# Kernel optimization log

Measured on AMD Instinct MI355X. Metric: run time of the kernel, lower is better.

## Reference

```python
import jax, jax.numpy as jnp
import numpy as np

EPS = 1e-5
KP_EXTENT = 0.05


def _lrelu(x):
    return jnp.where(x >= 0, x, 0.1 * x)


def _bn(x, g, b, m, v):
    return g * (x - m) * jax.lax.rsqrt(v + EPS) + b


def setup_inputs() -> dict:
    key = jax.random.key(0)
    ks = jax.random.split(key, 20)
    N, K, P = 40000, 32, 15
    C_in, mid, C_out = 128, 64, 256
    inp = {}
    inp["features"] = jax.random.normal(ks[0], (N, C_in), dtype=jnp.float32)
    # points in a small cube so neighbor distances ~ KP_radius (0.06)
    inp["points"] = jax.random.uniform(ks[1], (N, 3), dtype=jnp.float32) * 0.1
    inp["neighbor_idx"] = jax.random.randint(ks[2], (N, K), 0, N, dtype=jnp.int32)
    # main path: Conv1D(in->mid) + BN
    inp["W1"] = jax.random.normal(ks[3], (C_in, mid), dtype=jnp.float32) * (1.0 / np.sqrt(C_in))
    inp["bn1_g"] = 1.0 + 0.1 * jax.random.normal(ks[4], (mid,), dtype=jnp.float32)
    inp["bn1_b"] = 0.1 * jax.random.normal(ks[5], (mid,), dtype=jnp.float32)
    inp["bn1_m"] = 0.1 * jax.random.normal(ks[6], (mid,), dtype=jnp.float32)
    inp["bn1_v"] = 0.5 + 0.5 * jax.random.uniform(ks[7], (mid,), dtype=jnp.float32)
    # KPConv: fixed kernel point positions in ball of radius 0.06, weights [P, mid, mid]
    inp["kernel_points"] = jax.random.normal(ks[8], (P, 3), dtype=jnp.float32) * 0.03
    inp["Wkp"] = jax.random.normal(ks[9], (P, mid, mid), dtype=jnp.float32) * (1.0 / np.sqrt(P * mid))
    # Conv1D(mid->out) + BN
    inp["W2"] = jax.random.normal(ks[10], (mid, C_out), dtype=jnp.float32) * (1.0 / np.sqrt(mid))
    inp["bn2_g"] = 1.0 + 0.1 * jax.random.normal(ks[11], (C_out,), dtype=jnp.float32)
    inp["bn2_b"] = 0.1 * jax.random.normal(ks[12], (C_out,), dtype=jnp.float32)
    inp["bn2_m"] = 0.1 * jax.random.normal(ks[13], (C_out,), dtype=jnp.float32)
    inp["bn2_v"] = 0.5 + 0.5 * jax.random.uniform(ks[14], (C_out,), dtype=jnp.float32)
    # shortcut Conv1D(in->out) + BN
    inp["Ws"] = jax.random.normal(ks[15], (C_in, C_out), dtype=jnp.float32) * (1.0 / np.sqrt(C_in))
    inp["bns_g"] = 1.0 + 0.1 * jax.random.normal(ks[16], (C_out,), dtype=jnp.float32)
    inp["bns_b"] = 0.1 * jax.random.normal(ks[17], (C_out,), dtype=jnp.float32)
    inp["bns_m"] = 0.1 * jax.random.normal(ks[18], (C_out,), dtype=jnp.float32)
    inp["bns_v"] = 0.5 + 0.5 * jax.random.uniform(ks[19], (C_out,), dtype=jnp.float32)
    return inp


def reference(features, points, neighbor_idx,
              W1, bn1_g, bn1_b, bn1_m, bn1_v,
              kernel_points, Wkp,
              W2, bn2_g, bn2_b, bn2_m, bn2_v,
              Ws, bns_g, bns_b, bns_m, bns_v):
    # --- main path ---
    # Conv1D: pointwise linear + BN(eval) + LeakyReLU
    x = _lrelu(_bn(features @ W1, bn1_g, bn1_b, bn1_m, bn1_v))  # [N, mid]
    # KPConvNeighbors (rigid KPConv, linear influence)
    f_n = x[neighbor_idx]                                # [N, K, mid] gather
    d = points[neighbor_idx] - points[:, None, :]        # [N, K, 3]
    diff = d[:, :, None, :] - kernel_points[None, None]  # [N, K, P, 3]
    dist = jnp.sqrt(jnp.sum(diff * diff, axis=-1))       # [N, K, P]
    h = jnp.maximum(0.0, 1.0 - dist / KP_EXTENT)         # influence [N, K, P]
    wf = jnp.einsum('nkp,nkc->npc', h, f_n)              # [N, P, mid]
    y = jnp.einsum('npc,pcd->nd', wf, Wkp)               # [N, mid]
    y = _lrelu(y)
    y = _lrelu(_bn(y @ W2, bn2_g, bn2_b, bn2_m, bn2_v))  # [N, C_out]
    # --- shortcut ---
    sc = _lrelu(_bn(features @ Ws, bns_g, bns_b, bns_m, bns_v))
    # residual add + final leaky relu
    return _lrelu(y + sc)
```

## Files before the change

kernel.cpp:

```cpp
#include <hip/hip_runtime.h>
#include <math.h>

#define EPSBN 1e-5f

constexpr int CIN  = 128;
constexpr int MID  = 64;
constexpr int COUT = 256;
constexpr int KNB  = 32;
constexpr int PKP  = 15;

constexpr int PSTR = 72;
constexpr int WROW = PKP * PSTR;
constexpr int YROW = 72;

typedef __bf16 v8bf  __attribute__((ext_vector_type(8)));
typedef float  f32x4 __attribute__((ext_vector_type(4)));

__device__ __forceinline__ float lrelu(float x) { return x >= 0.0f ? x : 0.1f * x; }

__device__ __forceinline__ void split1(float v, unsigned short& h, unsigned short& l) {
    __bf16 hb = (__bf16)v;
    float r = v - (float)hb;
    __bf16 lb = (__bf16)r;
    h = __builtin_bit_cast(unsigned short, hb);
    l = __builtin_bit_cast(unsigned short, lb);
}

__device__ __forceinline__ void split_frag8(const float* s, v8bf& hi, v8bf& lo) {
    #pragma unroll
    for (int j = 0; j < 8; ++j) {
        __bf16 hb = (__bf16)s[j];
        float r = s[j] - (float)hb;
        hi[j] = hb;
        lo[j] = (__bf16)r;
    }
}

__device__ __forceinline__ v8bf as_v8bf(uint4 u) {
    union { uint4 u; v8bf v; } X;
    X.u = u;
    return X.v;
}

__device__ __forceinline__ unsigned bf16_rne(float f) {
    unsigned u = __float_as_uint(f);
    return (u + 0x7fffu + ((u >> 16) & 1u)) >> 16;
}
__device__ __forceinline__ void split_pack8(const float* s, v8bf& hi, v8bf& lo) {
    unsigned h[8], l[8];
    #pragma unroll
    for (int j = 0; j < 8; ++j) {
        float a = s[j];
        unsigned hu = bf16_rne(a);
        float r = a - __uint_as_float(hu << 16);
        h[j] = hu;
        l[j] = bf16_rne(r);
    }
    union { uint4 u; v8bf v; } H, L;
    H.u = make_uint4(h[0] | (h[1] << 16), h[2] | (h[3] << 16),
                     h[4] | (h[5] << 16), h[6] | (h[7] << 16));
    L.u = make_uint4(l[0] | (l[1] << 16), l[2] | (l[3] << 16),
                     l[4] | (l[5] << 16), l[6] | (l[7] << 16));
    hi = H.v;
    lo = L.v;
}

__global__ __launch_bounds__(256) void prep(
    const float* __restrict__ Wkp, const float* __restrict__ W1,
    const float* __restrict__ Ws,  const float* __restrict__ W2,
    const float* __restrict__ g1, const float* __restrict__ b1,
    const float* __restrict__ m1, const float* __restrict__ v1,
    const float* __restrict__ gs, const float* __restrict__ bs,
    const float* __restrict__ ms, const float* __restrict__ vs,
    const float* __restrict__ g2, const float* __restrict__ b2,
    const float* __restrict__ m2, const float* __restrict__ v2,
    uint4* __restrict__ WkpPh, uint4* __restrict__ WkpPl,
    uint4* __restrict__ WcPh,  uint4* __restrict__ WcPl,
    uint4* __restrict__ W2Ph,  uint4* __restrict__ W2Pl,
    float* __restrict__ bnscale, float* __restrict__ bnshift)
{
    const int b = blockIdx.x, t = threadIdx.x;
    if (b < 30) {
        int gt = b * 256 + t;
        int lane = gt & 63, rest = gt >> 6;
        int nt = rest & 3, kt = rest >> 2;
        int col = nt * 16 + (lane & 15);
        int kbase = kt * 32 + ((lane >> 4) << 3);
        float tmp[8];
        #pragma unroll
        for (int j = 0; j < 8; ++j)
            tmp[j] = Wkp[(size_t)(kbase + j) * MID + col];
        v8bf hi, lo;
        split_pack8(tmp, hi, lo);
        union { v8bf v; uint4 u; } H, L; H.v = hi; L.v = lo;
        WkpPh[gt] = H.u; WkpPl[gt] = L.u;
    } else if (b < 50) {
        int gt = (b - 30) * 256 + t;
        int lane = gt & 63, rest = gt >> 6;
        int kt = rest / 20, nt = rest % 20;
        int c = nt * 16 + (lane & 15);
        int kbase = kt * 32 + ((lane >> 4) << 3);
        float tmp[8];
        #pragma unroll
        for (int j = 0; j < 8; ++j) {
            int k = kbase + j;
            tmp[j] = (c < 64) ? W1[(size_t)k * MID + c]
                              : Ws[(size_t)k * COUT + (c - 64)];
        }
        v8bf hi, lo;
        split_pack8(tmp, hi, lo);
        union { v8bf v; uint4 u; } H, L; H.v = hi; L.v = lo;
        WcPh[gt] = H.u; WcPl[gt] = L.u;
    } else if (b < 58) {
        int gt = (b - 50) * 256 + t;
        int lane = gt & 63, rest = gt >> 6;
        int kt = rest >> 4, nt = rest & 15;
        int col = nt * 16 + (lane & 15);
        int kbase = kt * 32 + ((lane >> 4) << 3);
        float tmp[8];
        #pragma unroll
        for (int j = 0; j < 8; ++j)
            tmp[j] = W2[(size_t)(kbase + j) * COUT + col];
        v8bf hi, lo;
        split_pack8(tmp, hi, lo);
        union { v8bf v; uint4 u; } H, L; H.v = hi; L.v = lo;
        W2Ph[gt] = H.u; W2Pl[gt] = L.u;
    } else {
        int v = (b - 58) * 256 + t;
        if (v < 576) {
            float g, bb, mm, vv;
            if (v < 64)       { g = g1[v]; bb = b1[v]; mm = m1[v]; vv = v1[v]; }
            else if (v < 320) { int c = v - 64;  g = gs[c]; bb = bs[c]; mm = ms[c]; vv = vs[c]; }
            else              { int c = v - 320; g = g2[c]; bb = b2[c]; mm = m2[c]; vv = v2[c]; }
            float s = g / sqrtf(vv + EPSBN);
            bnscale[v] = s;
            bnshift[v] = bb - mm * s;
        }
    }
}

__global__ __launch_bounds__(256) void k1_mfma(
    const float* __restrict__ F,
    const uint4* __restrict__ WcPh, const uint4* __restrict__ WcPl,
    const float* __restrict__ bnscale, const float* __restrict__ bnshift,
    unsigned* __restrict__ xp, float* __restrict__ scbuf)
{
    const int t = threadIdx.x;
    const int l = t & 63, w = t >> 6;
    const int n0 = blockIdx.x * 64;
    const int ntbase = blockIdx.y * 10;
    const int colr = l & 15, kg = l >> 4;
    const int arow = n0 + w * 16 + colr;
    const int k8 = kg * 8;

    const float* fr = F + (size_t)arow * CIN + k8;
    float4 av[4][2];
    #pragma unroll
    for (int kt = 0; kt < 4; ++kt) {
        av[kt][0] = *(const float4*)(fr + kt * 32);
        av[kt][1] = *(const float4*)(fr + kt * 32 + 4);
    }

    f32x4 acc[10];
    #pragma unroll
    for (int nt = 0; nt < 10; ++nt) acc[nt] = (f32x4){0.f, 0.f, 0.f, 0.f};

    #pragma unroll
    for (int kt = 0; kt < 4; ++kt) {
        float tmp[8] = {av[kt][0].x, av[kt][0].y, av[kt][0].z, av[kt][0].w,
                        av[kt][1].x, av[kt][1].y, av[kt][1].z, av[kt][1].w};
        v8bf ah, al;
        split_frag8(tmp, ah, al);
        #pragma unroll
        for (int nt = 0; nt < 10; ++nt) {
            int bidx = ((kt * 20 + ntbase + nt) << 6) + l;
            v8bf bh = as_v8bf(WcPh[bidx]);
            v8bf bl = as_v8bf(WcPl[bidx]);
            acc[nt] = __builtin_amdgcn_mfma_f32_16x16x32_bf16(ah, bh, acc[nt], 0, 0, 0);
            acc[nt] = __builtin_amdgcn_mfma_f32_16x16x32_bf16(al, bh, acc[nt], 0, 0, 0);
            acc[nt] = __builtin_amdgcn_mfma_f32_16x16x32_bf16(ah, bl, acc[nt], 0, 0, 0);
        }
    }

    const int rq = kg * 4;
    #pragma unroll
    for (int nt = 0; nt < 10; ++nt) {
        int col = (ntbase + nt) * 16 + colr;
        float sc = bnscale[col], sh = bnshift[col];
        #pragma unroll
        for (int r = 0; r < 4; ++r) {
            int row = n0 + w * 16 + rq + r;
            float val = lrelu(acc[nt][r] * sc + sh);
            if (col < 64) {
                unsigned short hu, lu;
                split1(val, hu, lu);
                xp[(size_t)row * MID + col] = ((unsigned)hu << 16) | lu;
            } else {
                scbuf[(size_t)row * COUT + (col - 64)] = val;
            }
        }
    }
}

__global__ __launch_bounds__(512) void k234_fused(
    const unsigned* __restrict__ xp,
    const float* __restrict__ pts,
    const int* __restrict__ nidx,
    const float* __restrict__ kpp,
    const uint4* __restrict__ WkpPh, const uint4* __restrict__ WkpPl,
    const uint4* __restrict__ W2Ph,  const uint4* __restrict__ W2Pl,
    const float* __restrict__ bnscale, const float* __restrict__ bnshift,
    const float* __restrict__ scbuf,
    float* __restrict__ out)
{
    __shared__ unsigned short wfsH[16 * WROW];
    __shared__ unsigned short wfsL[16 * WROW];
    __shared__ float         yP[4][16][17];
    __shared__ unsigned short yH[16 * YROW];
    __shared__ unsigned short yL[16 * YROW];

    const int t = threadIdx.x;
    const int l = t & 63, w = t >> 6;
    const int col = l & 15, kg = l >> 4;
    const int k8 = kg * 8;
    const int n0 = blockIdx.x * 16;

    float kx = 0.f, ky = 0.f, kz = 0.f;
    if (col < PKP) { kx = kpp[col * 3]; ky = kpp[col * 3 + 1]; kz = kpp[col * 3 + 2]; }

    for (int pt = 0; pt < 2; ++pt) {
        const int pl = w * 2 + pt;
        const int n  = n0 + pl;
        const float cx = pts[(size_t)n * 3];
        const float cy = pts[(size_t)n * 3 + 1];
        const float cz = pts[(size_t)n * 3 + 2];
        const int4 nba = ((const int4*)nidx)[(size_t)n * 8 + kg * 2];
        const int4 nbb = ((const int4*)nidx)[(size_t)n * 8 + kg * 2 + 1];
        int nb[8] = {nba.x, nba.y, nba.z, nba.w, nbb.x, nbb.y, nbb.z, nbb.w};

        unsigned u[8][4];
        #pragma unroll
        for (int j = 0; j < 8; ++j) {
            const unsigned* xr = xp + (size_t)nb[j] * MID + col;
            u[j][0] = xr[0];
            u[j][1] = xr[16];
            u[j][2] = xr[32];
            u[j][3] = xr[48];
        }

        float hv[8];
        #pragma unroll
        for (int j = 0; j < 8; ++j) {
            float ex = (pts[(size_t)nb[j] * 3]     - cx) - kx;
            float ey = (pts[(size_t)nb[j] * 3 + 1] - cy) - ky;
            float ez = (pts[(size_t)nb[j] * 3 + 2] - cz) - kz;
            float dist = sqrtf(ex * ex + ey * ey + ez * ez);
            float h = fmaxf(0.0f, 1.0f - dist * 20.0f);
            hv[j] = (col < PKP) ? h : 0.0f;
        }
        v8bf ah, al;
        split_frag8(hv, ah, al);

        #pragma unroll
        for (int nt = 0; nt < 4; ++nt) {
            unsigned bhW[4], blW[4];
            #pragma unroll
            for (int i = 0; i < 4; ++i) {
                unsigned u0 = u[2 * i][nt], u1 = u[2 * i + 1][nt];
                bhW[i] = (u1 & 0xFFFF0000u) | (u0 >> 16);
                blW[i] = (u1 << 16) | (u0 & 0xFFFFu);
            }
            v8bf bh = as_v8bf(make_uint4(bhW[0], bhW[1], bhW[2], bhW[3]));
            v8bf bl = as_v8bf(make_uint4(blW[0], blW[1], blW[2], blW[3]));
            f32x4 acc = {0.f, 0.f, 0.f, 0.f};
            acc = __builtin_amdgcn_mfma_f32_16x16x32_bf16(ah, bh, acc, 0, 0, 0);
            acc = __builtin_amdgcn_mfma_f32_16x16x32_bf16(al, bh, acc, 0, 0, 0);
            acc = __builtin_amdgcn_mfma_f32_16x16x32_bf16(ah, bl, acc, 0, 0, 0);
            #pragma unroll
            for (int r = 0; r < 4; ++r) {
                int p = kg * 4 + r;
                if (p < PKP) {
                    unsigned short hu, lu;
                    split1(acc[r], hu, lu);
                    int off = pl * WROW + p * PSTR + nt * 16 + col;
                    wfsH[off] = hu;
                    wfsL[off] = lu;
                }
            }
        }
    }
    __syncthreads();

    const int nt = w & 3;
    const int khalf = w >> 2;
    f32x4 a0 = {0.f, 0.f, 0.f, 0.f};
    f32x4 a1 = {0.f, 0.f, 0.f, 0.f};
    f32x4 a2 = {0.f, 0.f, 0.f, 0.f};
    #pragma unroll
    for (int i = 0; i < 15; ++i) {
        int kt = khalf * 15 + i;
        int koff = col * WROW + (kt >> 1) * PSTR + (kt & 1) * 32 + k8;
        v8bf ah = as_v8bf(*(const uint4*)&wfsH[koff]);
        v8bf al = as_v8bf(*(const uint4*)&wfsL[koff]);
        int bidx = ((kt << 2) + nt) * 64 + l;
        v8bf bh = as_v8bf(WkpPh[bidx]);
        v8bf bl = as_v8bf(WkpPl[bidx]);
        a0 = __builtin_amdgcn_mfma_f32_16x16x32_bf16(ah, bh, a0, 0, 0, 0);
        a1 = __builtin_amdgcn_mfma_f32_16x16x32_bf16(al, bh, a1, 0, 0, 0);
        a2 = __builtin_amdgcn_mfma_f32_16x16x32_bf16(ah, bl, a2, 0, 0, 0);
    }
    if (khalf == 1) {
        #pragma unroll
        for (int r = 0; r < 4; ++r)
            yP[nt][kg * 4 + r][col] = a0[r] + a1[r] + a2[r];
    }
    __syncthreads();
    if (khalf == 0) {
        #pragma unroll
        for (int r = 0; r < 4; ++r) {
            float yv = lrelu(a0[r] + a1[r] + a2[r] + yP[nt][kg * 4 + r][col]);
            unsigned short hu, lu;
            split1(yv, hu, lu);
            int off = (kg * 4 + r) * YROW + nt * 16 + col;
            yH[off] = hu;
            yL[off] = lu;
        }
    }
    __syncthreads();

    f32x4 acc2[2];
    #pragma unroll
    for (int i = 0; i < 2; ++i) acc2[i] = (f32x4){0.f, 0.f, 0.f, 0.f};
    #pragma unroll
    for (int kt = 0; kt < 2; ++kt) {
        int yoff = col * YROW + kt * 32 + k8;
        v8bf ah = as_v8bf(*(const uint4*)&yH[yoff]);
        v8bf al = as_v8bf(*(const uint4*)&yL[yoff]);
        #pragma unroll
        for (int ii = 0; ii < 2; ++ii) {
            int nt2 = w * 2 + ii;
            int bidx = (((kt << 4) + nt2) << 6) + l;
            v8bf bh = as_v8bf(W2Ph[bidx]);
            v8bf bl = as_v8bf(W2Pl[bidx]);
            acc2[ii] = __builtin_amdgcn_mfma_f32_16x16x32_bf16(ah, bh, acc2[ii], 0, 0, 0);
            acc2[ii] = __builtin_amdgcn_mfma_f32_16x16x32_bf16(al, bh, acc2[ii], 0, 0, 0);
            acc2[ii] = __builtin_amdgcn_mfma_f32_16x16x32_bf16(ah, bl, acc2[ii], 0, 0, 0);
        }
    }
    #pragma unroll
    for (int ii = 0; ii < 2; ++ii) {
        int cold = (w * 2 + ii) * 16 + col;
        float sc = bnscale[320 + cold], sh = bnshift[320 + cold];
        #pragma unroll
        for (int r = 0; r < 4; ++r) {
            int n = n0 + kg * 4 + r;
            float val = lrelu(acc2[ii][r] * sc + sh);
            float scv = scbuf[(size_t)n * COUT + cold];
            out[(size_t)n * COUT + cold] = lrelu(val + scv);
        }
    }
}

extern "C" void kernel_launch(void* const* d_in, const int* in_sizes, int n_in,
                              void* d_out, int out_size, void* d_ws, size_t ws_size,
                              hipStream_t stream)
{
    const float* F   = (const float*)d_in[0];
    const float* pts = (const float*)d_in[1];
    const int*   nid = (const int*)d_in[2];
    const float* W1  = (const float*)d_in[3];
    const float* g1  = (const float*)d_in[4];
    const float* b1  = (const float*)d_in[5];
    const float* m1  = (const float*)d_in[6];
    const float* v1  = (const float*)d_in[7];
    const float* kpp = (const float*)d_in[8];
    const float* Wkp = (const float*)d_in[9];
    const float* W2  = (const float*)d_in[10];
    const float* g2  = (const float*)d_in[11];
    const float* b2  = (const float*)d_in[12];
    const float* m2  = (const float*)d_in[13];
    const float* v2  = (const float*)d_in[14];
    const float* Ws  = (const float*)d_in[15];
    const float* gs  = (const float*)d_in[16];
    const float* bs  = (const float*)d_in[17];
    const float* ms  = (const float*)d_in[18];
    const float* vs  = (const float*)d_in[19];

    const int N = in_sizes[0] / CIN;

    unsigned* xp   = (unsigned*)d_ws;
    float* scbuf   = (float*)(xp + (size_t)N * MID);
    uint4* WkpPh   = (uint4*)(scbuf + (size_t)N * COUT);
    uint4* WkpPl   = WkpPh + 7680;
    uint4* WcPh    = WkpPl + 7680;
    uint4* WcPl    = WcPh + 5120;
    uint4* W2Ph    = WcPl + 5120;
    uint4* W2Pl    = W2Ph + 2048;
    float* bnscale = (float*)(W2Pl + 2048);
    float* bnshift = bnscale + 576;
    float* out     = (float*)d_out;

    prep<<<61, 256, 0, stream>>>(Wkp, W1, Ws, W2,
                                 g1, b1, m1, v1, gs, bs, ms, vs, g2, b2, m2, v2,
                                 WkpPh, WkpPl, WcPh, WcPl, W2Ph, W2Pl,
                                 bnscale, bnshift);
    k1_mfma<<<dim3(N / 64, 2), 256, 0, stream>>>(F, WcPh, WcPl, bnscale, bnshift, xp, scbuf);
    k234_fused<<<N / 16, 512, 0, stream>>>(xp, pts, nid, kpp,
                                           WkpPh, WkpPl, W2Ph, W2Pl,
                                           bnscale, bnshift, scbuf, out);
}
```

Measured before the change: 220.9 us.

## Fuse shortcut GEMM into final kernel and vectorize neighbor feature gather

Moves the shortcut Conv1D (features @ Ws with BN and LeakyReLU) out of the first kernel and into the fused KPConv kernel. This removes the N x 256 float shortcut buffer round-trip through global memory, and the first kernel now only computes the 64-wide W1 projection. The intermediate x is stored in an interleaved layout, so each neighbor's features can be gathered with a single uint4 load instead of four strided loads. Byte-permute intrinsics replace the shift/mask repacking. In exchange, the fused kernel must reload the input features and run extra MFMAs, which raises register pressure.

New measurement: 257.0 us. 1.16x slower.

```diff
diff --git a/kernel.cpp b/kernel.cpp
--- a/kernel.cpp
+++ b/kernel.cpp
@@ -75,7 +75,8 @@
     const float* __restrict__ g2, const float* __restrict__ b2,
     const float* __restrict__ m2, const float* __restrict__ v2,
     uint4* __restrict__ WkpPh, uint4* __restrict__ WkpPl,
-    uint4* __restrict__ WcPh,  uint4* __restrict__ WcPl,
+    uint4* __restrict__ W1Ph,  uint4* __restrict__ W1Pl,
+    uint4* __restrict__ WsPh,  uint4* __restrict__ WsPl,
     uint4* __restrict__ W2Ph,  uint4* __restrict__ W2Pl,
     float* __restrict__ bnscale, float* __restrict__ bnshift)
 {
@@ -94,23 +95,34 @@
         split_pack8(tmp, hi, lo);
         union { v8bf v; uint4 u; } H, L; H.v = hi; L.v = lo;
         WkpPh[gt] = H.u; WkpPl[gt] = L.u;
-    } else if (b < 50) {
+    } else if (b < 34) {
         int gt = (b - 30) * 256 + t;
         int lane = gt & 63, rest = gt >> 6;
-        int kt = rest / 20, nt = rest % 20;
-        int c = nt * 16 + (lane & 15);
+        int kt = rest >> 2, nt = rest & 3;
+        int col = nt * 16 + (lane & 15);
         int kbase = kt * 32 + ((lane >> 4) << 3);
         float tmp[8];
         #pragma unroll
-        for (int j = 0; j < 8; ++j) {
-            int k = kbase + j;
-            tmp[j] = (c < 64) ? W1[(size_t)k * MID + c]
-                              : Ws[(size_t)k * COUT + (c - 64)];
-        }
+        for (int j = 0; j < 8; ++j)
+            tmp[j] = W1[(size_t)(kbase + j) * MID + col];
         v8bf hi, lo;
         split_pack8(tmp, hi, lo);
         union { v8bf v; uint4 u; } H, L; H.v = hi; L.v = lo;
-        WcPh[gt] = H.u; WcPl[gt] = L.u;
+        W1Ph[gt] = H.u; W1Pl[gt] = L.u;
+    } else if (b < 50) {
+        int gt = (b - 34) * 256 + t;
+        int lane = gt & 63, rest = gt >> 6;
+        int kt = rest >> 4, nt = rest & 15;
+        int col = nt * 16 + (lane & 15);
+        int kbase = kt * 32 + ((lane >> 4) << 3);
+        float tmp[8];
+        #pragma unroll
+        for (int j = 0; j < 8; ++j)
+            tmp[j] = Ws[(size_t)(kbase + j) * COUT + col];
+        v8bf hi, lo;
+        split_pack8(tmp, hi, lo);
+        union { v8bf v; uint4 u; } H, L; H.v = hi; L.v = lo;
+        WsPh[gt] = H.u; WsPl[gt] = L.u;
     } else if (b < 58) {
         int gt = (b - 50) * 256 + t;
         int lane = gt & 63, rest = gt >> 6;
@@ -141,14 +153,13 @@
 
 __global__ __launch_bounds__(256) void k1_mfma(
     const float* __restrict__ F,
-    const uint4* __restrict__ WcPh, const uint4* __restrict__ WcPl,
+    const uint4* __restrict__ W1Ph, const uint4* __restrict__ W1Pl,
     const float* __restrict__ bnscale, const float* __restrict__ bnshift,
-    unsigned* __restrict__ xp, float* __restrict__ scbuf)
+    unsigned* __restrict__ xp)
 {
     const int t = threadIdx.x;
     const int l = t & 63, w = t >> 6;
     const int n0 = blockIdx.x * 64;
-    const int ntbase = blockIdx.y * 10;
     const int colr = l & 15, kg = l >> 4;
     const int arow = n0 + w * 16 + colr;
     const int k8 = kg * 8;
@@ -161,9 +172,9 @@
         av[kt][1] = *(const float4*)(fr + kt * 32 + 4);
     }
 
-    f32x4 acc[10];
-    #pragma unroll
-    for (int nt = 0; nt < 10; ++nt) acc[nt] = (f32x4){0.f, 0.f, 0.f, 0.f};
+    f32x4 acc[4];
+    #pragma unroll
+    for (int nt = 0; nt < 4; ++nt) acc[nt] = (f32x4){0.f, 0.f, 0.f, 0.f};
 
     #pragma unroll
     for (int kt = 0; kt < 4; ++kt) {
@@ -172,32 +183,27 @@
         v8bf ah, al;
         split_frag8(tmp, ah, al);
         #pragma unroll
-        for (int nt = 0; nt < 10; ++nt) {
-            int bidx = ((kt * 20 + ntbase + nt) << 6) + l;
-            v8bf bh = as_v8bf(WcPh[bidx]);
-            v8bf bl = as_v8bf(WcPl[bidx]);
+        for (int nt = 0; nt < 4; ++nt) {
+            int bidx = (((kt << 2) + nt) << 6) + l;
+            v8bf bh = as_v8bf(W1Ph[bidx]);
+            v8bf bl = as_v8bf(W1Pl[bidx]);
             acc[nt] = __builtin_amdgcn_mfma_f32_16x16x32_bf16(ah, bh, acc[nt], 0, 0, 0);
             acc[nt] = __builtin_amdgcn_mfma_f32_16x16x32_bf16(al, bh, acc[nt], 0, 0, 0);
             acc[nt] = __builtin_amdgcn_mfma_f32_16x16x32_bf16(ah, bl, acc[nt], 0, 0, 0);
         }
     }
 
-    const int rq = kg * 4;
-    #pragma unroll
-    for (int nt = 0; nt < 10; ++nt) {
-        int col = (ntbase + nt) * 16 + colr;
+    #pragma unroll
+    for (int nt = 0; nt < 4; ++nt) {
+        int col = nt * 16 + colr;
         float sc = bnscale[col], sh = bnshift[col];
         #pragma unroll
         for (int r = 0; r < 4; ++r) {
-            int row = n0 + w * 16 + rq + r;
+            int row = n0 + w * 16 + kg * 4 + r;
             float val = lrelu(acc[nt][r] * sc + sh);
-            if (col < 64) {
-                unsigned short hu, lu;
-                split1(val, hu, lu);
-                xp[(size_t)row * MID + col] = ((unsigned)hu << 16) | lu;
-            } else {
-                scbuf[(size_t)row * COUT + (col - 64)] = val;
-            }
+            unsigned short hu, lu;
+            split1(val, hu, lu);
+            xp[(size_t)row * MID + colr * 4 + nt] = ((unsigned)hu << 16) | lu;
         }
     }
 }
@@ -207,10 +213,11 @@
     const float* __restrict__ pts,
     const int* __restrict__ nidx,
     const float* __restrict__ kpp,
+    const float* __restrict__ F,
     const uint4* __restrict__ WkpPh, const uint4* __restrict__ WkpPl,
     const uint4* __restrict__ W2Ph,  const uint4* __restrict__ W2Pl,
+    const uint4* __restrict__ WsPh,  const uint4* __restrict__ WsPl,
     const float* __restrict__ bnscale, const float* __restrict__ bnshift,
-    const float* __restrict__ scbuf,
     float* __restrict__ out)
 {
     __shared__ unsigned short wfsH[16 * WROW];
@@ -225,9 +232,18 @@
     const int k8 = kg * 8;
     const int n0 = blockIdx.x * 16;
 
+    const float* frS = F + (size_t)(n0 + col) * CIN + k8;
+    float4 fS[4][2];
+    #pragma unroll
+    for (int kt = 0; kt < 4; ++kt) {
+        fS[kt][0] = *(const float4*)(frS + kt * 32);
+        fS[kt][1] = *(const float4*)(frS + kt * 32 + 4);
+    }
+
     float kx = 0.f, ky = 0.f, kz = 0.f;
     if (col < PKP) { kx = kpp[col * 3]; ky = kpp[col * 3 + 1]; kz = kpp[col * 3 + 2]; }
 
+    #pragma unroll
     for (int pt = 0; pt < 2; ++pt) {
         const int pl = w * 2 + pt;
         const int n  = n0 + pl;
@@ -241,11 +257,8 @@
         unsigned u[8][4];
         #pragma unroll
         for (int j = 0; j < 8; ++j) {
-            const unsigned* xr = xp + (size_t)nb[j] * MID + col;
-            u[j][0] = xr[0];
-            u[j][1] = xr[16];
-            u[j][2] = xr[32];
-            u[j][3] = xr[48];
+            uint4 X = ((const uint4*)(xp + (size_t)nb[j] * MID))[col];
+            u[j][0] = X.x; u[j][1] = X.y; u[j][2] = X.z; u[j][3] = X.w;
         }
 
         float hv[8];
@@ -267,8 +280,8 @@
             #pragma unroll
             for (int i = 0; i < 4; ++i) {
                 unsigned u0 = u[2 * i][nt], u1 = u[2 * i + 1][nt];
-                bhW[i] = (u1 & 0xFFFF0000u) | (u0 >> 16);
-                blW[i] = (u1 << 16) | (u0 & 0xFFFFu);
+                bhW[i] = __builtin_amdgcn_perm(u1, u0, 0x07060302u);
+                blW[i] = __builtin_amdgcn_perm(u1, u0, 0x05040100u);
             }
             v8bf bh = as_v8bf(make_uint4(bhW[0], bhW[1], bhW[2], bhW[3]));
             v8bf bl = as_v8bf(make_uint4(blW[0], blW[1], blW[2], blW[3]));
@@ -328,9 +341,29 @@
     }
     __syncthreads();
 
-    f32x4 acc2[2];
-    #pragma unroll
-    for (int i = 0; i < 2; ++i) acc2[i] = (f32x4){0.f, 0.f, 0.f, 0.f};
+    f32x4 acc2[2], accS[2];
+    #pragma unroll
+    for (int i = 0; i < 2; ++i) {
+        acc2[i] = (f32x4){0.f, 0.f, 0.f, 0.f};
+        accS[i] = (f32x4){0.f, 0.f, 0.f, 0.f};
+    }
+    #pragma unroll
+    for (int kt = 0; kt < 4; ++kt) {
+        float tmp[8] = {fS[kt][0].x, fS[kt][0].y, fS[kt][0].z, fS[kt][0].w,
+                        fS[kt][1].x, fS[kt][1].y, fS[kt][1].z, fS[kt][1].w};
+        v8bf ah, al;
+        split_frag8(tmp, ah, al);
+        #pragma unroll
+        for (int ii = 0; ii < 2; ++ii) {
+            int nt2 = w * 2 + ii;
+            int bidx = (((kt << 4) + nt2) << 6) + l;
+            v8bf bh = as_v8bf(WsPh[bidx]);
+            v8bf bl = as_v8bf(WsPl[bidx]);
+            accS[ii] = __builtin_amdgcn_mfma_f32_16x16x32_bf16(ah, bh, accS[ii], 0, 0, 0);
+            accS[ii] = __builtin_amdgcn_mfma_f32_16x16x32_bf16(al, bh, accS[ii], 0, 0, 0);
+            accS[ii] = __builtin_amdgcn_mfma_f32_16x16x32_bf16(ah, bl, accS[ii], 0, 0, 0);
+        }
+    }
     #pragma unroll
     for (int kt = 0; kt < 2; ++kt) {
         int yoff = col * YROW + kt * 32 + k8;
@@ -350,13 +383,14 @@
     #pragma unroll
     for (int ii = 0; ii < 2; ++ii) {
         int cold = (w * 2 + ii) * 16 + col;
-        float sc = bnscale[320 + cold], sh = bnshift[320 + cold];
+        float sc2 = bnscale[320 + cold], sh2 = bnshift[320 + cold];
+        float scS = bnscale[64 + cold],  shS = bnshift[64 + cold];
         #pragma unroll
         for (int r = 0; r < 4; ++r) {
             int n = n0 + kg * 4 + r;
-            float val = lrelu(acc2[ii][r] * sc + sh);
-            float scv = scbuf[(size_t)n * COUT + cold];
-            out[(size_t)n * COUT + cold] = lrelu(val + scv);
+            float mainv = lrelu(acc2[ii][r] * sc2 + sh2);
+            float scv   = lrelu(accS[ii][r] * scS + shS);
+            out[(size_t)n * COUT + cold] = lrelu(mainv + scv);
         }
     }
 }
@@ -389,12 +423,13 @@
     const int N = in_sizes[0] / CIN;
 
     unsigned* xp   = (unsigned*)d_ws;
-    float* scbuf   = (float*)(xp + (size_t)N * MID);
-    uint4* WkpPh   = (uint4*)(scbuf + (size_t)N * COUT);
+    uint4* WkpPh   = (uint4*)(xp + (size_t)N * MID);
     uint4* WkpPl   = WkpPh + 7680;
-    uint4* WcPh    = WkpPl + 7680;
-    uint4* WcPl    = WcPh + 5120;
-    uint4* W2Ph    = WcPl + 5120;
+    uint4* W1Ph    = WkpPl + 7680;
+    uint4* W1Pl    = W1Ph + 1024;
+    uint4* WsPh    = W1Pl + 1024;
+    uint4* WsPl    = WsPh + 4096;
+    uint4* W2Ph    = WsPl + 4096;
     uint4* W2Pl    = W2Ph + 2048;
     float* bnscale = (float*)(W2Pl + 2048);
     float* bnshift = bnscale + 576;
@@ -402,10 +437,10 @@
 
     prep<<<61, 256, 0, stream>>>(Wkp, W1, Ws, W2,
                                  g1, b1, m1, v1, gs, bs, ms, vs, g2, b2, m2, v2,
-                                 WkpPh, WkpPl, WcPh, WcPl, W2Ph, W2Pl,
+                                 WkpPh, WkpPl, W1Ph, W1Pl, WsPh, WsPl, W2Ph, W2Pl,
                                  bnscale, bnshift);
-    k1_mfma<<<dim3(N / 64, 2), 256, 0, stream>>>(F, WcPh, WcPl, bnscale, bnshift, xp, scbuf);
-    k234_fused<<<N / 16, 512, 0, stream>>>(xp, pts, nid, kpp,
-                                           WkpPh, WkpPl, W2Ph, W2Pl,
-                                           bnscale, bnshift, scbuf, out);
-}
+    k1_mfma<<<N / 64, 256, 0, stream>>>(F, W1Ph, W1Pl, bnscale, bnshift, xp);
+    k234_fused<<<N / 16, 512, 0, stream>>>(xp, pts, nid, kpp, F,
+                                           WkpPh, WkpPl, W2Ph, W2Pl, WsPh, WsPl,
+                                           bnscale, bnshift, out);
+}
```
